# Kernel tuning notes

Measured on AMD Instinct MI355X. Metric: run time of the kernel, lower is better.

## Reference

```python
import jax, jax.numpy as jnp
import numpy as np

N_HEADS = 8


def setup_inputs() -> dict:
    key = jax.random.key(0)
    ks = jax.random.split(key, 6)
    B, T, D = 8192, 64, 128
    s = 1.0 / np.sqrt(D)
    return {
        "center": jax.random.normal(ks[0], (B, D), dtype=jnp.float32),
        "neighbors": jax.random.normal(ks[1], (B, T, D), dtype=jnp.float32),
        "W_Q": jax.random.normal(ks[2], (D, D), dtype=jnp.float32) * s,
        "W_K": jax.random.normal(ks[3], (D, D), dtype=jnp.float32) * s,
        "W_V": jax.random.normal(ks[4], (D, D), dtype=jnp.float32) * s,
        "W_O": jax.random.normal(ks[5], (D, D), dtype=jnp.float32) * s,
    }


def reference(center, neighbors, W_Q, W_K, W_V, W_O):
    # center: [B, D], neighbors: [B, T, D]
    B, D = center.shape
    H = N_HEADS
    hd = D // H
    scale = hd ** -0.5
    # tokens = [center] ++ neighbors -> [B, 1+T, D]
    tokens = jnp.concatenate([center[:, None, :], neighbors], axis=1)
    # Only the center row of the attention output is used, so only the
    # center query is needed (math identical to the torch module's out[:, 0]).
    q = (center @ W_Q).reshape(B, H, hd)                 # [B, H, hd]
    K = (tokens @ W_K).reshape(B, -1, H, hd)             # [B, 1+T, H, hd]
    V = (tokens @ W_V).reshape(B, -1, H, hd)             # [B, 1+T, H, hd]
    scores = jnp.einsum('bhd,bthd->bht', q, K) * scale   # [B, H, 1+T]
    attn = jax.nn.softmax(scores, axis=-1)
    out = jnp.einsum('bht,bthd->bhd', attn, V).reshape(B, D)
    return out @ W_O
```

## Files before the change

kernel.cpp:

```cpp
#include <hip/hip_runtime.h>
#include <hip/hip_bf16.h>
#include <math.h>

namespace {

constexpr int D  = 128;
constexpr int TN = 64;
constexpr int NB = 8;

typedef _Float16 h2 __attribute__((ext_vector_type(2)));

__device__ __forceinline__ unsigned pack_h2(float a, float b) {
    h2 v; v.x = (_Float16)a; v.y = (_Float16)b;
    return __builtin_bit_cast(unsigned, v);
}
__device__ __forceinline__ float2 unp_h2(unsigned u) {
    h2 v = __builtin_bit_cast(h2, u);
    return make_float2((float)v.x, (float)v.y);
}
__device__ __forceinline__ h2 bch2(unsigned u) { return __builtin_bit_cast(h2, u); }
__device__ __forceinline__ float fdot2f(unsigned a, unsigned b, float c) {
#if __has_builtin(__builtin_amdgcn_fdot2)
    return __builtin_amdgcn_fdot2(__builtin_bit_cast(h2, a),
                                  __builtin_bit_cast(h2, b), c, false);
#else
    const float2 fa = unp_h2(a), fb = unp_h2(b);
    return fmaf(fa.x, fb.x, fmaf(fa.y, fb.y, c));
#endif
}


__global__ __launch_bounds__(256)
void k0_nm(const float* __restrict__ WQ, const float* __restrict__ WK,
           const float* __restrict__ WV, const float* __restrict__ WO,
           unsigned* __restrict__ N2, unsigned* __restrict__ M2)
{
    const int t = blockIdx.x * 256 + threadIdx.x;
    {
        const int kk = t >> 10, col = t & 1023;
        const int h = col >> 7, d = col & 127;
        const float* wq0 = WQ + (size_t)(2 * kk) * D + h * 16;
        const float* wq1 = wq0 + D;
        const float* wk  = WK + (size_t)d * D + h * 16;
        float a0 = 0.f, a1 = 0.f;
        #pragma unroll
        for (int j = 0; j < 16; ++j) {
            a0 = fmaf(wq0[j], wk[j], a0);
            a1 = fmaf(wq1[j], wk[j], a1);
        }
        N2[t] = pack_h2(0.25f * a0, 0.25f * a1);
    }
    {
        const int kk = t >> 7, e = t & 127;
        const int k0 = 2 * kk;
        const int h = k0 >> 7, d = k0 & 127;
        const float* wv0 = WV + (size_t)d * D + h * 16;
        const float* wv1 = wv0 + D;
        const float* wo  = WO + (size_t)(h * 16) * D + e;
        float b0 = 0.f, b1 = 0.f;
        #pragma unroll
        for (int j = 0; j < 16; ++j) {
            const float w_ = wo[(size_t)j * D];
            b0 = fmaf(wv0[j], w_, b0);
            b1 = fmaf(wv1[j], w_, b1);
        }
        M2[t] = pack_h2(b0, b1);
    }
}

__global__ __launch_bounds__(256, 2)
void k_fused(const float* __restrict__ center, const float* __restrict__ neighbors,
             const unsigned* __restrict__ N2, const unsigned* __restrict__ M2,
             float* __restrict__ out)
{
    __shared__ __align__(16) float nb_lds[TN * D / 2];
    __shared__ __align__(16) float qs8f[NB * 512];
    __shared__ __align__(16) unsigned c2u[NB * 64];
    __shared__ __align__(16) unsigned Pu[TN * 12];
    __shared__ float red_pc[8];

    const int tid = threadIdx.x;
    const int w   = tid >> 6;
    const int l   = tid & 63;
    const size_t rb = (size_t)blockIdx.x * NB;

    uint2* nbu  = (uint2*)nb_lds;
    uint2* qs8u = (uint2*)qs8f;

    {
        const int r = tid >> 5, f = tid & 31;
        const float4 g = ((const float4*)(center + (rb + r) * (size_t)D))[f];
        c2u[r * 64 + 2 * f]     = pack_h2(g.x, g.y);
        c2u[r * 64 + 2 * f + 1] = pack_h2(g.z, g.w);
    }
    __syncthreads();

    {
        const uint4* N2u4 = (const uint4*)N2;
        float4 acc[NB];
        #pragma unroll
        for (int r = 0; r < NB; ++r) acc[r] = make_float4(0.f, 0.f, 0.f, 0.f);

        #pragma unroll 2
        for (int kk2 = 0; kk2 < 32; ++kk2) {
            const int kk = 2 * kk2;
            const uint4 ua = N2u4[(size_t)kk * 256 + tid];
            const uint4 ub = N2u4[(size_t)(kk + 1) * 256 + tid];
            #pragma unroll
            for (int r = 0; r < NB; ++r) {
                const uint2 cp = *reinterpret_cast<const uint2*>(&c2u[r * 64 + kk]);
                acc[r].x = fdot2f(cp.x, ua.x, acc[r].x);
                acc[r].y = fdot2f(cp.x, ua.y, acc[r].y);
                acc[r].z = fdot2f(cp.x, ua.z, acc[r].z);
                acc[r].w = fdot2f(cp.x, ua.w, acc[r].w);
                acc[r].x = fdot2f(cp.y, ub.x, acc[r].x);
                acc[r].y = fdot2f(cp.y, ub.y, acc[r].y);
                acc[r].z = fdot2f(cp.y, ub.z, acc[r].z);
                acc[r].w = fdot2f(cp.y, ub.w, acc[r].w);
            }
        }
        const int fc = tid & 31;
        const int qslot = (tid & ~31) | (((fc & 7) << 2) | (fc >> 3));
        #pragma unroll
        for (int r = 0; r < NB; ++r)
            qs8u[r * 256 + qslot] =
                make_uint2(pack_h2(acc[r].x, acc[r].y), pack_h2(acc[r].z, acc[r].w));
    }

    float4 st[8];
    {
        const float4* g0 = (const float4*)(neighbors + rb * TN * D);
        #pragma unroll
        for (int i = 0; i < 8; ++i) st[i] = g0[i * 256 + tid];
    }
    __syncthreads();

    #pragma unroll 1
    for (int bb = 0; bb < NB; ++bb) {
        #pragma unroll
        for (int i = 0; i < 8; ++i) {
            const int fi = i * 256 + tid;
            const int t  = fi >> 5;
            const int fc = fi & 31;
            nbu[(t << 5) | (fc ^ (t & 7))] =
                make_uint2(pack_h2(st[i].x, st[i].y), pack_h2(st[i].z, st[i].w));
        }
        __syncthreads();

        if (bb + 1 < NB) {
            const float4* gn = (const float4*)(neighbors + (rb + bb + 1) * TN * D);
            #pragma unroll
            for (int i = 0; i < 8; ++i) st[i] = gn[i * 256 + tid];
        }

        const uint2*    nb2 = (const uint2*)nb_lds;
        const uint2*    qku = qs8u + bb * 256;
        const unsigned* cb2 = c2u + bb * 64;

        const int tg = l & 15;
        const int q  = l >> 4;
        const int h0 = 2 * w;

        unsigned cr[16];
        {
            const uint4* cb4 = (const uint4*)(cb2 + q * 16);
            *reinterpret_cast<uint4*>(&cr[0])  = cb4[0];
            *reinterpret_cast<uint4*>(&cr[4])  = cb4[1];
            *reinterpret_cast<uint4*>(&cr[8])  = cb4[2];
            *reinterpret_cast<uint4*>(&cr[12]) = cb4[3];
        }

        float sc0[4] = {0.f, 0.f, 0.f, 0.f};
        float sc1[4] = {0.f, 0.f, 0.f, 0.f};
        float s0a = 0.f, s0b = 0.f;
        #pragma unroll
        for (int jj = 0; jj < 8; ++jj) {
            const int rfc = (jj << 2) | q;
            const int fc  = (q << 3) | jj;
            const uint2 kv0p = qku[h0 * 32 + rfc];
            const uint2 kv1p = qku[(h0 + 1) * 32 + rfc];
            const unsigned cpa = cr[2 * jj], cpb = cr[2 * jj + 1];
            s0a = fdot2f(cpa, kv0p.x, fdot2f(cpb, kv0p.y, s0a));
            s0b = fdot2f(cpa, kv1p.x, fdot2f(cpb, kv1p.y, s0b));
            #pragma unroll
            for (int k = 0; k < 4; ++k) {
                const int t = tg + (k << 4);
                const uint2 u = nb2[(t << 5) | (fc ^ (t & 7))];
                sc0[k] = fdot2f(u.x, kv0p.x, fdot2f(u.y, kv0p.y, sc0[k]));
                sc1[k] = fdot2f(u.x, kv1p.x, fdot2f(u.y, kv1p.y, sc1[k]));
            }
        }
        #pragma unroll
        for (int k = 0; k < 4; ++k) {
            sc0[k] += __shfl_xor(sc0[k], 16);  sc0[k] += __shfl_xor(sc0[k], 32);
            sc1[k] += __shfl_xor(sc1[k], 16);  sc1[k] += __shfl_xor(sc1[k], 32);
        }
        s0a += __shfl_xor(s0a, 16);  s0a += __shfl_xor(s0a, 32);
        s0b += __shfl_xor(s0b, 16);  s0b += __shfl_xor(s0b, 32);

        float m0 = fmaxf(fmaxf(sc0[0], sc0[1]), fmaxf(sc0[2], sc0[3]));
        float m1 = fmaxf(fmaxf(sc1[0], sc1[1]), fmaxf(sc1[2], sc1[3]));
        #pragma unroll
        for (int off = 8; off >= 1; off >>= 1) {
            m0 = fmaxf(m0, __shfl_xor(m0, off));
            m1 = fmaxf(m1, __shfl_xor(m1, off));
        }
        m0 = fmaxf(m0, s0a);
        m1 = fmaxf(m1, s0b);
        float e0v[4], e1v[4];
        float sum0 = 0.f, sum1 = 0.f;
        #pragma unroll
        for (int k = 0; k < 4; ++k) {
            e0v[k] = __expf(sc0[k] - m0);  sum0 += e0v[k];
            e1v[k] = __expf(sc1[k] - m1);  sum1 += e1v[k];
        }
        #pragma unroll
        for (int off = 8; off >= 1; off >>= 1) {
            sum0 += __shfl_xor(sum0, off);
            sum1 += __shfl_xor(sum1, off);
        }
        const float ec0 = __expf(s0a - m0);
        const float ec1 = __expf(s0b - m1);
        const float inv0 = 1.0f / (sum0 + ec0);
        const float inv1 = 1.0f / (sum1 + ec1);
        if (q == 0) {
            #pragma unroll
            for (int k = 0; k < 4; ++k) {
                const int t = tg + (k << 4);
                const float p0 = e0v[k] * inv0;
                const float p1 = e1v[k] * inv1;
                *reinterpret_cast<uint2*>(&Pu[t * 12 + h0]) =
                    make_uint2(pack_h2(p0, p0), pack_h2(p1, p1));
            }
            if (tg == 0) {
                red_pc[h0]     = ec0 * inv0;
                red_pc[h0 + 1] = ec1 * inv1;
            }
        }
        __syncthreads();

        const int hl  = l >> 5;
        const int fc2 = l & 31;
        h2 pk00 = {0, 0}, pk01 = {0, 0};
        h2 pk10 = {0, 0}, pk11 = {0, 0};
        h2 pk20 = {0, 0}, pk21 = {0, 0};
        h2 pk30 = {0, 0}, pk31 = {0, 0};
        #pragma unroll
        for (int tt = 0; tt < 16; ++tt) {
            const int t = w * 16 + tt;
            const uint2 u = nb2[(t << 5) | (fc2 ^ (t & 7))];
            const h2 u0 = bch2(u.x), u1 = bch2(u.y);
            const uint4 pp = *reinterpret_cast<const uint4*>(&Pu[t * 12 + hl * 4]);
            const h2 p0 = bch2(pp.x), p1 = bch2(pp.y), p2 = bch2(pp.z), p3 = bch2(pp.w);
            pk00 += p0 * u0;  pk01 += p0 * u1;
            pk10 += p1 * u0;  pk11 += p1 * u1;
            pk20 += p2 * u0;  pk21 += p2 * u1;
            pk30 += p3 * u0;  pk31 += p3 * u1;
        }
        {
            float4 pf;
            pf = make_float4((float)pk00.x, (float)pk00.y, (float)pk01.x, (float)pk01.y);
            ((float4*)nb_lds)[w * 256 + (hl * 4 + 0) * 32 + fc2] = pf;
            pf = make_float4((float)pk10.x, (float)pk10.y, (float)pk11.x, (float)pk11.y);
            ((float4*)nb_lds)[w * 256 + (hl * 4 + 1) * 32 + fc2] = pf;
            pf = make_float4((float)pk20.x, (float)pk20.y, (float)pk21.x, (float)pk21.y);
            ((float4*)nb_lds)[w * 256 + (hl * 4 + 2) * 32 + fc2] = pf;
            pf = make_float4((float)pk30.x, (float)pk30.y, (float)pk31.x, (float)pk31.y);
            ((float4*)nb_lds)[w * 256 + (hl * 4 + 3) * 32 + fc2] = pf;
        }
        __syncthreads();

        {
            const int hE = tid >> 5;
            const int fE = tid & 31;
            float4 sum = make_float4(0.f, 0.f, 0.f, 0.f);
            #pragma unroll
            for (int ww = 0; ww < 4; ++ww) {
                const float4 p = ((const float4*)nb_lds)[ww * 256 + hE * 32 + fE];
                sum.x += p.x; sum.y += p.y; sum.z += p.z; sum.w += p.w;
            }
            const float pc = red_pc[hE];
            const float2 ca = unp_h2(cb2[2 * fE]), cb = unp_h2(cb2[2 * fE + 1]);
            sum.x = fmaf(pc, ca.x, sum.x);
            sum.y = fmaf(pc, ca.y, sum.y);
            sum.z = fmaf(pc, cb.x, sum.z);
            sum.w = fmaf(pc, cb.y, sum.w);
            qs8u[bb * 256 + tid] =
                make_uint2(pack_h2(sum.x, sum.y), pack_h2(sum.z, sum.w));
        }
        __syncthreads();
    }

    {
        const int cg = tid & 31;
        const int kg = tid >> 5;
        const int c4i = cg << 2;
        const int kb2 = kg << 6;

        float4 acc[NB];
        #pragma unroll
        for (int r = 0; r < NB; ++r) acc[r] = make_float4(0.f, 0.f, 0.f, 0.f);

        const uint4* M2u4 = (const uint4*)M2;
        const unsigned* sp2 = (const unsigned*)qs8f;

        #pragma unroll 2
        for (int k4 = 0; k4 < 32; ++k4) {
            const int kk = kb2 + 2 * k4;
            const uint4 ua = M2u4[(size_t)kk * 32 + cg];
            const uint4 ub = M2u4[(size_t)(kk + 1) * 32 + cg];
            #pragma unroll
            for (int r = 0; r < NB; ++r) {
                const uint2 sv = *reinterpret_cast<const uint2*>(&sp2[r * 512 + kk]);
                acc[r].x = fdot2f(sv.x, ua.x, acc[r].x);
                acc[r].y = fdot2f(sv.x, ua.y, acc[r].y);
                acc[r].z = fdot2f(sv.x, ua.z, acc[r].z);
                acc[r].w = fdot2f(sv.x, ua.w, acc[r].w);
                acc[r].x = fdot2f(sv.y, ub.x, acc[r].x);
                acc[r].y = fdot2f(sv.y, ub.y, acc[r].y);
                acc[r].z = fdot2f(sv.y, ub.z, acc[r].z);
                acc[r].w = fdot2f(sv.y, ub.w, acc[r].w);
            }
        }
        __syncthreads();
        float* baseW = (kg < 4) ? nb_lds : qs8f;
        const int kgm = kg & 3;
        #pragma unroll
        for (int r = 0; r < NB; ++r)
            *reinterpret_cast<float4*>(&baseW[(kgm * 8 + r) * 128 + c4i]) = acc[r];
        __syncthreads();

        {
            const int r = tid >> 5;
            float4 sum = make_float4(0.f, 0.f, 0.f, 0.f);
            #pragma unroll
            for (int g = 0; g < 8; ++g) {
                const float* bg = (g < 4) ? nb_lds : qs8f;
                const float4 p = *reinterpret_cast<const float4*>(
                    &bg[((g & 3) * 8 + r) * 128 + c4i]);
                sum.x += p.x; sum.y += p.y; sum.z += p.z; sum.w += p.w;
            }
            *reinterpret_cast<float4*>(out + (rb + r) * D + c4i) = sum;
        }
    }
}

}

extern "C" void kernel_launch(void* const* d_in, const int* in_sizes, int n_in,
                              void* d_out, int out_size, void* d_ws, size_t ws_size,
                              hipStream_t stream) {
    const float* center    = (const float*)d_in[0];
    const float* neighbors = (const float*)d_in[1];
    const float* WQ        = (const float*)d_in[2];
    const float* WK        = (const float*)d_in[3];
    const float* WV        = (const float*)d_in[4];
    const float* WO        = (const float*)d_in[5];
    float* outp            = (float*)d_out;

    const int B = in_sizes[0] / D;

    unsigned* N2 = (unsigned*)d_ws;
    unsigned* M2 = N2 + 64 * 1024;

    hipLaunchKernelGGL(k0_nm,   dim3(256),    dim3(256), 0, stream, WQ, WK, WV, WO, N2, M2);
    hipLaunchKernelGGL(k_fused, dim3(B / NB), dim3(256), 0, stream, center, neighbors, N2, M2, outp);
}
```

Baseline: 101.8 us.

## Restructure P·V so each wave owns its heads and drops cross-wave reduction

The attention-weighted sum over neighbor tokens is reorganized so each wave handles its own two heads across all 64 tokens, instead of every wave covering a 16-token slice of all heads. This removes the partial-sum round trip through shared memory, two block-wide barriers and the red_pc buffer, relying on an intra-wave LDS wait instead. In exchange each wave does more sequential LDS reads of neighbor data, and the accumulation now stays in fp16 over all 64 tokens plus the center term, which may lose precision.

```diff
diff --git a/kernel.cpp b/kernel.cpp
--- a/kernel.cpp
+++ b/kernel.cpp
@@ -19,6 +19,7 @@
     return make_float2((float)v.x, (float)v.y);
 }
 __device__ __forceinline__ h2 bch2(unsigned u) { return __builtin_bit_cast(h2, u); }
+__device__ __forceinline__ unsigned bcu(h2 v) { return __builtin_bit_cast(unsigned, v); }
 __device__ __forceinline__ float fdot2f(unsigned a, unsigned b, float c) {
 #if __has_builtin(__builtin_amdgcn_fdot2)
     return __builtin_amdgcn_fdot2(__builtin_bit_cast(h2, a),
@@ -76,8 +77,7 @@
     __shared__ __align__(16) float nb_lds[TN * D / 2];
     __shared__ __align__(16) float qs8f[NB * 512];
     __shared__ __align__(16) unsigned c2u[NB * 64];
-    __shared__ __align__(16) unsigned Pu[TN * 12];
-    __shared__ float red_pc[8];
+    __shared__ __align__(16) unsigned Pu[8 * 64];
 
     const int tid = threadIdx.x;
     const int w   = tid >> 6;
@@ -223,70 +223,59 @@
         const float ec1 = __expf(s0b - m1);
         const float inv0 = 1.0f / (sum0 + ec0);
         const float inv1 = 1.0f / (sum1 + ec1);
+        const float pctr0 = ec0 * inv0;
+        const float pctr1 = ec1 * inv1;
         if (q == 0) {
             #pragma unroll
             for (int k = 0; k < 4; ++k) {
                 const int t = tg + (k << 4);
                 const float p0 = e0v[k] * inv0;
                 const float p1 = e1v[k] * inv1;
-                *reinterpret_cast<uint2*>(&Pu[t * 12 + h0]) =
-                    make_uint2(pack_h2(p0, p0), pack_h2(p1, p1));
-            }
-            if (tg == 0) {
-                red_pc[h0]     = ec0 * inv0;
-                red_pc[h0 + 1] = ec1 * inv1;
-            }
-        }
-        __syncthreads();
-
-        const int hl  = l >> 5;
-        const int fc2 = l & 31;
-        h2 pk00 = {0, 0}, pk01 = {0, 0};
-        h2 pk10 = {0, 0}, pk11 = {0, 0};
-        h2 pk20 = {0, 0}, pk21 = {0, 0};
-        h2 pk30 = {0, 0}, pk31 = {0, 0};
-        #pragma unroll
-        for (int tt = 0; tt < 16; ++tt) {
-            const int t = w * 16 + tt;
-            const uint2 u = nb2[(t << 5) | (fc2 ^ (t & 7))];
-            const h2 u0 = bch2(u.x), u1 = bch2(u.y);
-            const uint4 pp = *reinterpret_cast<const uint4*>(&Pu[t * 12 + hl * 4]);
-            const h2 p0 = bch2(pp.x), p1 = bch2(pp.y), p2 = bch2(pp.z), p3 = bch2(pp.w);
-            pk00 += p0 * u0;  pk01 += p0 * u1;
-            pk10 += p1 * u0;  pk11 += p1 * u1;
-            pk20 += p2 * u0;  pk21 += p2 * u1;
-            pk30 += p3 * u0;  pk31 += p3 * u1;
-        }
+                Pu[h0 * 64 + t]       = pack_h2(p0, p0);
+                Pu[(h0 + 1) * 64 + t] = pack_h2(p1, p1);
+            }
+        }
+        asm volatile("s_waitcnt lgkmcnt(0)" ::: "memory");
+
         {
-            float4 pf;
-            pf = make_float4((float)pk00.x, (float)pk00.y, (float)pk01.x, (float)pk01.y);
-            ((float4*)nb_lds)[w * 256 + (hl * 4 + 0) * 32 + fc2] = pf;
-            pf = make_float4((float)pk10.x, (float)pk10.y, (float)pk11.x, (float)pk11.y);
-            ((float4*)nb_lds)[w * 256 + (hl * 4 + 1) * 32 + fc2] = pf;
-            pf = make_float4((float)pk20.x, (float)pk20.y, (float)pk21.x, (float)pk21.y);
-            ((float4*)nb_lds)[w * 256 + (hl * 4 + 2) * 32 + fc2] = pf;
-            pf = make_float4((float)pk30.x, (float)pk30.y, (float)pk31.x, (float)pk31.y);
-            ((float4*)nb_lds)[w * 256 + (hl * 4 + 3) * 32 + fc2] = pf;
-        }
-        __syncthreads();
-
-        {
-            const int hE = tid >> 5;
-            const int fE = tid & 31;
-            float4 sum = make_float4(0.f, 0.f, 0.f, 0.f);
-            #pragma unroll
-            for (int ww = 0; ww < 4; ++ww) {
-                const float4 p = ((const float4*)nb_lds)[ww * 256 + hE * 32 + fE];
-                sum.x += p.x; sum.y += p.y; sum.z += p.z; sum.w += p.w;
-            }
-            const float pc = red_pc[hE];
-            const float2 ca = unp_h2(cb2[2 * fE]), cb = unp_h2(cb2[2 * fE + 1]);
-            sum.x = fmaf(pc, ca.x, sum.x);
-            sum.y = fmaf(pc, ca.y, sum.y);
-            sum.z = fmaf(pc, cb.x, sum.z);
-            sum.w = fmaf(pc, cb.y, sum.w);
-            qs8u[bb * 256 + tid] =
-                make_uint2(pack_h2(sum.x, sum.y), pack_h2(sum.z, sum.w));
+            const int hh  = l >> 5;
+            const int fc2 = l & 31;
+            const unsigned* Ph = Pu + (h0 + hh) * 64;
+            h2 a01 = {0, 0}, a23 = {0, 0};
+            #pragma unroll
+            for (int tt = 0; tt < 64; tt += 4) {
+                const uint4 pq = *reinterpret_cast<const uint4*>(&Ph[tt]);
+                {
+                    const int t = tt;
+                    const uint2 u = nb2[(t << 5) | (fc2 ^ (t & 7))];
+                    const h2 p = bch2(pq.x);
+                    a01 += p * bch2(u.x);  a23 += p * bch2(u.y);
+                }
+                {
+                    const int t = tt + 1;
+                    const uint2 u = nb2[(t << 5) | (fc2 ^ (t & 7))];
+                    const h2 p = bch2(pq.y);
+                    a01 += p * bch2(u.x);  a23 += p * bch2(u.y);
+                }
+                {
+                    const int t = tt + 2;
+                    const uint2 u = nb2[(t << 5) | (fc2 ^ (t & 7))];
+                    const h2 p = bch2(pq.z);
+                    a01 += p * bch2(u.x);  a23 += p * bch2(u.y);
+                }
+                {
+                    const int t = tt + 3;
+                    const uint2 u = nb2[(t << 5) | (fc2 ^ (t & 7))];
+                    const h2 p = bch2(pq.w);
+                    a01 += p * bch2(u.x);  a23 += p * bch2(u.y);
+                }
+            }
+            const float pcv = hh ? pctr1 : pctr0;
+            h2 pch; pch.x = (_Float16)pcv; pch.y = (_Float16)pcv;
+            const uint2 cc = *reinterpret_cast<const uint2*>(&cb2[2 * fc2]);
+            a01 += pch * bch2(cc.x);
+            a23 += pch * bch2(cc.y);
+            qs8u[bb * 256 + (h0 + hh) * 32 + fc2] = make_uint2(bcu(a01), bcu(a23));
         }
         __syncthreads();
     }
```

Measured after the change: 104.7 us. 2.8% more time.
